# Kernel optimization log

Measured on AMD Instinct MI355X. Metric: run time of the kernel, lower is better.

The kernel has to match this reference:

```python
import jax, jax.numpy as jnp
import numpy as np

Q_PTS = jnp.array([0.0, 0.25, 0.5, 0.75, 1.0], dtype=jnp.float32)
LN_EPS = 1e-5


def _lower_median(s):
    # torch.median returns the LOWER of the two middle values for even n
    return s[..., (s.shape[-1] - 1) // 2]


def _quantile_sorted(s, q):
    # torch.quantile default 'linear' interpolation, computed on pre-sorted s
    n = s.shape[-1]
    idx = q * (n - 1)
    lo = jnp.floor(idx).astype(jnp.int32)
    hi = jnp.ceil(idx).astype(jnp.int32)
    frac = (idx - lo).astype(s.dtype)
    return jnp.take(s, lo, axis=-1) * (1.0 - frac) + jnp.take(s, hi, axis=-1) * frac


def _robust_stats(flat):
    # flat: [L-1, B, N] -> [L-1, B, 7]  (median, MAD, 5 quantiles)
    s = jnp.sort(flat, axis=-1)
    med = _lower_median(s)[..., None]
    mad = _lower_median(jnp.sort(jnp.abs(flat - med), axis=-1))[..., None]
    q = _quantile_sorted(s, Q_PTS)
    return jnp.concatenate([med, mad, q], axis=-1)


def _layer_norm(x, eps=LN_EPS):
    mu = x.mean(-1, keepdims=True)
    var = ((x - mu) ** 2).mean(-1, keepdims=True)
    return (x - mu) * jax.lax.rsqrt(var + eps)


def _forward(ws, bs, fc1_w, fc1_b, ln_w, ln_b, gate_w, gate_b, fco_w, fco_b, scale):
    Lm1, B = ws.shape[0], ws.shape[1]
    w_flat = ws.reshape(Lm1, B, -1)
    b_flat = bs.reshape(Lm1, B, -1)
    w_feats = _robust_stats(w_flat)            # [L-1, B, 7]
    b_feats = _robust_stats(b_flat)            # [L-1, B, 7]
    g_mean = w_flat.mean(-1, keepdims=True)    # [L-1, B, 1]
    g_mad = jnp.zeros_like(g_mean)             # MAD over a size-1 axis is exactly 0
    combined = jnp.concatenate([w_feats, b_feats, g_mean, g_mad], axis=-1)  # [L-1, B, 16]
    x = _layer_norm(combined)                  # F.layer_norm without affine
    # ResidualMLP (vectorized over the layer axis l)
    h = jnp.einsum('lbi,lhi->lbh', x, fc1_w) + fc1_b[:, None, :]
    h = _layer_norm(h) * ln_w[:, None, :] + ln_b[:, None, :]
    h = jax.nn.gelu(h, approximate=False)      # nn.GELU() default = exact erf
    gate = jax.nn.sigmoid(jnp.einsum('lbh,lgh->lbg', h, gate_w) + gate_b[:, None, :])
    raw = jnp.einsum('lbg,log->lbo', h * gate, fco_w) + fco_b[:, None, :]
    return jnp.sin(raw) * scale[:, None, None] + 1.0   # [L-1, B, out_dim]


def setup_inputs() -> dict:
    key = jax.random.key(0)
    ks = jax.random.split(key, 8)
    Lm1, B, D, H, F_IN = 3, 64, 512, 64, 16
    return {
        'ws': jax.random.normal(ks[0], (Lm1, B, D, D), jnp.float32) * 0.05,
        'bs': jax.random.normal(ks[1], (Lm1, B, D), jnp.float32) * 0.05,
        'w_last': jax.random.normal(ks[2], (B, D, D), jnp.float32) * 0.05,
        'b_last': jax.random.normal(ks[3], (B, D), jnp.float32) * 0.05,
        'fc1_w': jax.random.normal(ks[4], (Lm1, H, F_IN), jnp.float32) * 0.2,
        'fc1_b': jnp.zeros((Lm1, H), jnp.float32),
        'ln_w': jnp.ones((Lm1, H), jnp.float32),
        'ln_b': jnp.zeros((Lm1, H), jnp.float32),
        'gate_w': jax.random.normal(ks[5], (Lm1, H, H), jnp.float32) * 0.15,
        'gate_b': jnp.zeros((Lm1, H), jnp.float32),
        'fco_w': jax.random.normal(ks[6], (Lm1, D, H), jnp.float32) * 0.1,
        'fco_b': jnp.zeros((Lm1, D), jnp.float32),
        'scale': jnp.full((Lm1,), 0.1, jnp.float32),
    }


def reference(ws, bs, w_last, b_last, fc1_w, fc1_b, ln_w, ln_b, gate_w, gate_b, fco_w, fco_b, scale):
    # w_last / b_last correspond to wsfeat[L-1]: received by forward but never used
    # (loop breaks at i == L-1), matching the torch module exactly.
    return _forward(ws, bs, fc1_w, fc1_b, ln_w, ln_b, gate_w, gate_b, fco_w, fco_b, scale)
```

## Files before the change

kernel.cpp:

```cpp
#include <hip/hip_runtime.h>
#include <cstdint>

#define NROW 192
#define NW   262144
#define NT   1024
#define QCAP 1024
#define SEGS_CAP 8192

__device__ __forceinline__ uint32_t mono(float x) {
    uint32_t u = __float_as_uint(x);
    return (u & 0x80000000u) ? ~u : (u | 0x80000000u);
}
__device__ __forceinline__ float unmono(uint32_t u) {
    uint32_t v = (u & 0x80000000u) ? (u & 0x7FFFFFFFu) : ~u;
    return __uint_as_float(v);
}
__device__ __forceinline__ int binof(float x, float lo, float s) {
    float d = (x - lo) * s;
    d = fminf(fmaxf(d, 0.0f), 4095.0f);
    return (int)d;
}

__device__ void block_select(const uint32_t* hist, int nb, uint32_t rank,
                             uint32_t* sbuf, volatile uint32_t* out, int tid) {
    int per = (nb + NT - 1) / NT;
    int base = tid * per;
    uint32_t s = 0;
    for (int i = 0; i < per; ++i) { int idx = base + i; if (idx < nb) s += hist[idx]; }
    uint32_t p = s;
    int lane = tid & 63;
    #pragma unroll
    for (int off = 1; off < 64; off <<= 1) {
        uint32_t v = __shfl_up(p, off);
        if (lane >= off) p += v;
    }
    int w = tid >> 6;
    if (lane == 63) sbuf[w] = p;
    __syncthreads();
    if (tid == 0) {
        uint32_t acc = 0;
        for (int i = 0; i < 16; ++i) { uint32_t t = sbuf[i]; sbuf[16 + i] = acc; acc += t; }
    }
    __syncthreads();
    uint32_t excl = sbuf[16 + w] + p - s;
    if (rank >= excl && rank < excl + s) {
        uint32_t rem = rank - excl;
        for (int i = 0; i < per; ++i) {
            int idx = base + i;
            if (idx >= nb) break;
            uint32_t c = hist[idx];
            if (rem < c) { out[0] = (uint32_t)idx; out[1] = rem; break; }
            rem -= c;
        }
    }
    __syncthreads();
}

__device__ uint32_t seg_select(const uint32_t* seg, uint32_t cnt, uint32_t rank,
                               uint32_t* hist2, uint32_t* sbuf,
                               volatile uint32_t* out2, int tid) {
    for (int i = tid; i < 2048; i += NT) hist2[i] = 0;
    __syncthreads();
    for (uint32_t i = tid; i < cnt; i += NT) atomicAdd(&hist2[seg[i] >> 21], 1u);
    __syncthreads();
    block_select(hist2, 2048, rank, sbuf, out2, tid);
    uint32_t b1 = out2[0], r1 = out2[1];
    __syncthreads();
    for (int i = tid; i < 2048; i += NT) hist2[i] = 0;
    __syncthreads();
    for (uint32_t i = tid; i < cnt; i += NT) {
        uint32_t k = seg[i];
        if ((k >> 21) == b1) atomicAdd(&hist2[(k >> 10) & 2047u], 1u);
    }
    __syncthreads();
    block_select(hist2, 2048, r1, sbuf, out2, tid);
    uint32_t b2 = out2[0], r2 = out2[1];
    __syncthreads();
    for (int i = tid; i < 1024; i += NT) hist2[i] = 0;
    __syncthreads();
    for (uint32_t i = tid; i < cnt; i += NT) {
        uint32_t k = seg[i];
        if ((k >> 21) == b1 && ((k >> 10) & 2047u) == b2)
            atomicAdd(&hist2[k & 1023u], 1u);
    }
    __syncthreads();
    block_select(hist2, 1024, r2, sbuf, out2, tid);
    uint32_t b3 = out2[0];
    __syncthreads();
    return (b1 << 21) + (b2 << 10) + b3;
}

__device__ uint32_t refine_global(const float4* p4, float med, int mode,
                                  uint32_t b1, uint32_t rem,
                                  uint32_t* hist2, uint32_t* sbuf,
                                  volatile uint32_t* out2, int tid) {
    for (int i = tid; i < 2048; i += NT) hist2[i] = 0;
    __syncthreads();
    for (int it = 0; it < 64; ++it) {
        float4 v = p4[tid + it * NT];
        float xs[4] = {v.x, v.y, v.z, v.w};
        #pragma unroll
        for (int c = 0; c < 4; ++c) {
            uint32_t u = mode ? __float_as_uint(fabsf(xs[c] - med)) : mono(xs[c]);
            if ((u >> 20) == b1) atomicAdd(&hist2[(u >> 9) & 2047u], 1u);
        }
    }
    __syncthreads();
    block_select(hist2, 2048, rem, sbuf, out2, tid);
    uint32_t b2 = out2[0], r2 = out2[1];
    __syncthreads();
    for (int i = tid; i < 512; i += NT) hist2[i] = 0;
    __syncthreads();
    for (int it = 0; it < 64; ++it) {
        float4 v = p4[tid + it * NT];
        float xs[4] = {v.x, v.y, v.z, v.w};
        #pragma unroll
        for (int c = 0; c < 4; ++c) {
            uint32_t u = mode ? __float_as_uint(fabsf(xs[c] - med)) : mono(xs[c]);
            if ((u >> 20) == b1 && ((u >> 9) & 2047u) == b2)
                atomicAdd(&hist2[u & 511u], 1u);
        }
    }
    __syncthreads();
    block_select(hist2, 512, r2, sbuf, out2, tid);
    uint32_t b3 = out2[0];
    __syncthreads();
    return (b1 << 20) + (b2 << 9) + b3;
}

__device__ void fb_path(const float4* p4, float* feat, int row,
                        uint32_t* hist, uint32_t* hist2, uint32_t* sbuf,
                        volatile uint32_t* out2, int tid) {
    const uint32_t RANK6[6] = {65535u, 65536u, 131071u, 131072u, 196607u, 196608u};
    for (int i = tid; i < 4096; i += NT) hist[i] = 0;
    __syncthreads();
    for (int it = 0; it < 64; ++it) {
        float4 v = p4[tid + it * NT];
        float xs[4] = {v.x, v.y, v.z, v.w};
        #pragma unroll
        for (int c = 0; c < 4; ++c) atomicAdd(&hist[mono(xs[c]) >> 20], 1u);
    }
    __syncthreads();
    uint32_t bins[6], rems[6];
    for (int k = 0; k < 6; ++k) {
        block_select(hist, 4096, RANK6[k], sbuf, out2, tid);
        bins[k] = out2[0]; rems[k] = out2[1];
        __syncthreads();
    }
    float svv[6];
    for (int k = 0; k < 6; ++k)
        svv[k] = unmono(refine_global(p4, 0.f, 0, bins[k], rems[k], hist2, sbuf, out2, tid));
    if (tid == 0) {
        float* f = feat + row * 16;
        f[0] = svv[2];
        f[3] = 0.25f * svv[0] + 0.75f * svv[1];
        f[4] = 0.5f  * (svv[2] + svv[3]);
        f[5] = 0.75f * svv[4] + 0.25f * svv[5];
    }
    float med = svv[2];
    __syncthreads();
    for (int i = tid; i < 4096; i += NT) hist[i] = 0;
    __syncthreads();
    for (int it = 0; it < 64; ++it) {
        float4 v = p4[tid + it * NT];
        float xs[4] = {v.x, v.y, v.z, v.w};
        #pragma unroll
        for (int c = 0; c < 4; ++c)
            atomicAdd(&hist[__float_as_uint(fabsf(xs[c] - med)) >> 20], 1u);
    }
    __syncthreads();
    block_select(hist, 4096, 131071u, sbuf, out2, tid);
    uint32_t mb = out2[0], mr = out2[1];
    __syncthreads();
    uint32_t mu = refine_global(p4, med, 1, mb, mr, hist2, sbuf, out2, tid);
    if (tid == 0) feat[row * 16 + 1] = __uint_as_float(mu);
}

__device__ __forceinline__ uint32_t Pv(const uint32_t* P, int k) {
    return (k >= 4096) ? (uint32_t)NW : P[k];
}
__device__ __forceinline__ uint32_t wup(float mL, float mR, float tau,
                                        float blo, float bsc, const uint32_t* P) {
    const int bR = binof(mR + tau, blo, bsc);
    const int bL = binof(mL - tau, blo, bsc);
    return Pv(P, bR + 1) - P[bL];
}
__device__ __forceinline__ uint32_t wlow(float mL, float mR, float tau,
                                         float blo, float bsc, const uint32_t* P) {
    const int bR = binof(mL + tau, blo, bsc);
    const int bL = binof(mR - tau, blo, bsc);
    const uint32_t a = P[bR];
    const uint32_t b = Pv(P, bL + 1);
    return (a > b) ? (a - b) : 0u;
}

__device__ void bitonic512g(float* a, int t2) {
    for (int k = 2; k <= 512; k <<= 1) {
        for (int j = k >> 1; j > 0; j >>= 1) {
            __syncthreads();
            for (int i = t2; i < 512; i += 256) {
                int ixj = i ^ j;
                if (ixj > i) {
                    float x = a[i], y = a[ixj];
                    bool up = ((i & k) == 0);
                    if ((x > y) == up) { a[i] = y; a[ixj] = x; }
                }
            }
        }
    }
    __syncthreads();
}

__global__ __launch_bounds__(NT) void stats_kernel(const float* __restrict__ wsrc,
                                                   const float* __restrict__ bsrc,
                                                   float* __restrict__ feat) {
    const int tid = threadIdx.x;
    __shared__ uint32_t hist[4096];
    __shared__ uint32_t sbuf[1024];
    __shared__ uint32_t segs[SEGS_CAP];
    __shared__ uint32_t ctrl[64];
    __shared__ float fctrl[8];

    if (blockIdx.x >= NROW) {
        const int g = tid >> 8, t2 = tid & 255;
        const int brow = (blockIdx.x - NROW) * 4 + g;
        float* a = ((float*)segs) + g * 512;
        float* d = ((float*)segs) + 2048 + g * 512;
        const float* p = bsrc + (size_t)brow * 512;
        for (int i = t2; i < 512; i += 256) a[i] = p[i];
        bitonic512g(a, t2);
        const float bmed = a[255];
        if (t2 == 0) {
            float* f = feat + brow * 16;
            f[7]  = bmed;
            f[9]  = a[0];
            f[10] = 0.25f * a[127] + 0.75f * a[128];
            f[11] = 0.5f  * (a[255] + a[256]);
            f[12] = 0.75f * a[383] + 0.25f * a[384];
            f[13] = a[511];
        }
        __syncthreads();
        for (int i = t2; i < 512; i += 256) d[i] = fabsf(a[i] - bmed);
        bitonic512g(d, t2);
        if (t2 == 0) feat[brow * 16 + 8] = d[255];
        return;
    }

    const int row = blockIdx.x;
    const float4* __restrict__ p4 = (const float4*)(wsrc + (size_t)row * NW);
    const int lane = tid & 63, wv = tid >> 6;
    float* fsb = (float*)sbuf;
    volatile uint32_t* out2 = (volatile uint32_t*)(ctrl + 62);

    {
        float smin = 1e30f, smax = -1e30f;
        #pragma unroll
        for (int k = 0; k < 8; ++k) {
            float4 v = p4[tid + k * NT];
            smin = fminf(smin, fminf(fminf(v.x, v.y), fminf(v.z, v.w)));
            smax = fmaxf(smax, fmaxf(fmaxf(v.x, v.y), fmaxf(v.z, v.w)));
        }
        #pragma unroll
        for (int off = 32; off > 0; off >>= 1) {
            smin = fminf(smin, __shfl_down(smin, off));
            smax = fmaxf(smax, __shfl_down(smax, off));
        }
        if (lane == 0) { fsb[wv * 2] = smin; fsb[wv * 2 + 1] = smax; }
        __syncthreads();
        if (tid == 0) {
            float mn = 1e30f, mx = -1e30f;
            for (int i = 0; i < 16; ++i) { mn = fminf(mn, fsb[i * 2]); mx = fmaxf(mx, fsb[i * 2 + 1]); }
            float span = mx - mn;
            float lo = mn - 0.0625f * span;
            float s = (span > 0.f) ? 4096.0f / (span * 1.125f) : 0.0f;
            fctrl[0] = lo; fctrl[1] = s;
        }
        __syncthreads();
    }
    const float blo = fctrl[0], bsc = fctrl[1];

    for (int i = tid; i < 4096; i += NT) hist[i] = 0;
    __syncthreads();
    {
        float sum = 0.f, fmn = 1e30f, fmx = -1e30f;
        for (int it = 0; it < 64; it += 8) {
            float4 a8[8];
            #pragma unroll
            for (int j = 0; j < 8; ++j) a8[j] = p4[tid + (it + j) * NT];
            #pragma unroll
            for (int j = 0; j < 8; ++j) {
                float xs[4] = {a8[j].x, a8[j].y, a8[j].z, a8[j].w};
                #pragma unroll
                for (int c = 0; c < 4; ++c) {
                    float x = xs[c];
                    sum += x;
                    fmn = fminf(fmn, x);
                    fmx = fmaxf(fmx, x);
                    atomicAdd(&hist[binof(x, blo, bsc)], 1u);
                }
            }
        }
        #pragma unroll
        for (int off = 32; off > 0; off >>= 1) {
            sum += __shfl_down(sum, off);
            fmn = fminf(fmn, __shfl_down(fmn, off));
            fmx = fmaxf(fmx, __shfl_down(fmx, off));
        }
        __syncthreads();
        if (lane == 0) { fsb[wv * 4] = sum; fsb[wv * 4 + 1] = fmn; fsb[wv * 4 + 2] = fmx; }
        __syncthreads();
        if (tid == 0) { float s = 0; for (int i = 0; i < 16; ++i) s += fsb[i * 4]; feat[row * 16 + 14] = s * (1.0f / (float)NW); }
        if (tid == 1) { float m = 1e30f;  for (int i = 0; i < 16; ++i) m = fminf(m, fsb[i * 4 + 1]); feat[row * 16 + 2] = m; fctrl[2] = m; }
        if (tid == 2) { float M = -1e30f; for (int i = 0; i < 16; ++i) M = fmaxf(M, fsb[i * 4 + 2]); feat[row * 16 + 6] = M; fctrl[3] = M; }
        if (tid == 3) feat[row * 16 + 15] = 0.0f;
        __syncthreads();
    }

    {
        const int b4 = tid * 4;
        const uint32_t v0 = hist[b4], v1 = hist[b4 + 1], v2 = hist[b4 + 2], v3 = hist[b4 + 3];
        const uint32_t s = v0 + v1 + v2 + v3;
        uint32_t p = s;
        #pragma unroll
        for (int off = 1; off < 64; off <<= 1) {
            uint32_t t = __shfl_up(p, off);
            if (lane >= off) p += t;
        }
        if (lane == 63) sbuf[wv] = p;
        __syncthreads();
        if (tid == 0) {
            uint32_t acc = 0;
            for (int i = 0; i < 16; ++i) { uint32_t t = sbuf[i]; sbuf[16 + i] = acc; acc += t; }
        }
        __syncthreads();
        const uint32_t excl = sbuf[16 + wv] + p - s;
        uint32_t ppA[5];
        ppA[0] = excl; ppA[1] = excl + v0; ppA[2] = ppA[1] + v1; ppA[3] = ppA[2] + v2; ppA[4] = ppA[3] + v3;
        hist[b4] = ppA[0]; hist[b4 + 1] = ppA[1]; hist[b4 + 2] = ppA[2]; hist[b4 + 3] = ppA[3];
        const uint32_t RANKS[6] = {65535u, 65536u, 131071u, 131072u, 196607u, 196608u};
        #pragma unroll
        for (int c = 0; c < 4; ++c) {
            #pragma unroll
            for (int q = 0; q < 6; ++q) {
                const uint32_t r = RANKS[q];
                if (ppA[c] <= r && r < ppA[c + 1]) {
                    ctrl[12 + q] = (uint32_t)(b4 + c);
                    ctrl[18 + q] = r - ppA[c];
                    ctrl[48 + q] = ppA[c + 1] - ppA[c];
                }
            }
        }
        __syncthreads();
    }

    if (tid == 0) {
        uint32_t ndl = 0, fail = 0;
        #pragma unroll
        for (int q = 0; q < 6; ++q) {
            const uint32_t b = ctrl[12 + q];
            int jf = -1;
            for (uint32_t t = 0; t < ndl; ++t) if (ctrl[24 + t] == b) { jf = (int)t; break; }
            if (jf < 0) {
                jf = (int)ndl;
                ctrl[24 + ndl] = b;
                ctrl[30 + ndl] = ctrl[48 + q];
                ndl++;
            }
            ctrl[36 + q] = (uint32_t)jf;
        }
        uint32_t off = 0;
        for (uint32_t t = 0; t < ndl; ++t) {
            ctrl[54 + t] = off;
            if (ctrl[30 + t] > QCAP) fail = 1;
            off += ctrl[30 + t];
        }
        if (off > 6144u) fail = 1;
        if (ctrl[14] == 0u || ctrl[14] == 4095u) fail = 1;
        ctrl[60] = off;
        ctrl[10] = ndl;
        ctrl[11] = fail;
        #pragma unroll
        for (int j = 0; j < 6; ++j) ctrl[j] = 0;
        ctrl[6] = 0;
        ctrl[7] = 0;
        ctrl[8] = 0;
        ctrl[9] = 0;
        ctrl[48] = 0xFFFFFFFFu; ctrl[49] = 0xFFFFFFFFu;
    }
    __syncthreads();
    if (ctrl[11]) { fb_path(p4, feat, row, hist, segs, sbuf, out2, tid); return; }

    const float wbin = 1.0f / bsc;
    const uint32_t m0 = ctrl[14];

    sbuf[tid] = 0;
    {
        const float mLf = blo + (float)m0 * wbin;
        const float mRf = mLf + wbin;
        #pragma unroll
        for (int c = 0; c < 4; ++c) {
            const int j = tid * 4 + c;
            const float tau = (float)j * wbin;
            const uint32_t up_j = wup(mLf, mRf, tau, blo, bsc, hist);
            if (up_j <= 131071u) {
                bool bnd = (j == 4095);
                if (!bnd) bnd = (wup(mLf, mRf, (float)(j + 1) * wbin, blo, bsc, hist) > 131071u);
                if (bnd) ctrl[48] = (uint32_t)j;
            }
            const uint32_t lo_j = wlow(mLf, mRf, tau, blo, bsc, hist);
            if (lo_j >= 131072u) {
                bool bnd = (j == 0);
                if (!bnd) bnd = (wlow(mLf, mRf, (float)(j - 1) * wbin, blo, bsc, hist) < 131072u);
                if (bnd) ctrl[49] = (uint32_t)j;
            }
        }
    }
    __syncthreads();
    if (tid < (int)ctrl[10]) ((uint8_t*)sbuf)[ctrl[24 + tid]] = (uint8_t)(tid + 1);
    const uint32_t jlo = ctrl[48], jhi = ctrl[49];
    float Awin = -1.0f;
    if (jlo != 0xFFFFFFFFu && jlo >= 2u) Awin = (float)(jlo - 2u) * wbin;
    float Bwin = (jhi == 0xFFFFFFFFu) ? 3.0e38f : (float)(jhi + 3u) * wbin;
    Bwin = fmaxf(Bwin, Awin + 3.0f * wbin);
    const float mtld = blo + ((float)m0 + 0.5f) * wbin;
    const uint32_t madbase = ctrl[60];
    __syncthreads();

    uint32_t myclo = 0;
    {
        const uint8_t* tbl = (const uint8_t*)sbuf;
        for (int it = 0; it < 64; it += 8) {
            float4 a8[8];
            #pragma unroll
            for (int j = 0; j < 8; ++j) a8[j] = p4[tid + (it + j) * NT];
            #pragma unroll
            for (int j = 0; j < 8; ++j) {
                float xs[4] = {a8[j].x, a8[j].y, a8[j].z, a8[j].w};
                #pragma unroll
                for (int c = 0; c < 4; ++c) {
                    float x = xs[c];
                    uint32_t m = tbl[binof(x, blo, bsc)];
                    if (m) {
                        uint32_t jj = m - 1u;
                        uint32_t pos = atomicAdd(&ctrl[jj], 1u);
                        if (pos < ctrl[30 + jj]) segs[ctrl[54 + jj] + pos] = mono(x);
                    }
                    float u = fabsf(x - mtld);
                    if (u <= Awin) myclo++;
                    else if (u <= Bwin) {
                        uint32_t pos = atomicAdd(&ctrl[6], 1u);
                        uint32_t slot = madbase + pos;
                        if (slot < SEGS_CAP) segs[slot] = __float_as_uint(x);
                    }
                }
            }
        }
    }
    __syncthreads();
    #pragma unroll
    for (int off = 32; off > 0; off >>= 1) myclo += __shfl_down(myclo, off);
    if (lane == 0) sbuf[wv] = myclo;
    __syncthreads();
    if (tid == 0) {
        uint32_t clo = 0;
        for (int i = 0; i < 16; ++i) clo += sbuf[i];
        ctrl[7] = clo;
        uint32_t fail = 0;
        const uint32_t ndl = ctrl[10];
        for (uint32_t j = 0; j < ndl; ++j) if (ctrl[j] != ctrl[30 + j]) fail = 1;
        if (ctrl[6] > SEGS_CAP - madbase) fail = 1;
        ctrl[11] = fail;
    }
    __syncthreads();
    if (ctrl[11]) { fb_path(p4, feat, row, hist, segs, sbuf, out2, tid); return; }

    {
        const uint32_t ndl = ctrl[10];
        for (uint32_t j = 0; j < ndl; ++j) {
            const uint32_t cnt = ctrl[j];
            const uint32_t base = ctrl[54 + j];
            if ((uint32_t)tid < cnt) {
                const uint32_t key = segs[base + tid];
                uint32_t r = 0;
                for (uint32_t i = 0; i < cnt; ++i) {
                    const uint32_t ki = segs[base + i];
                    r += (ki < key || (ki == key && i < (uint32_t)tid)) ? 1u : 0u;
                }
                #pragma unroll
                for (int q = 0; q < 6; ++q)
                    if (ctrl[36 + q] == j && ctrl[18 + q] == r) ctrl[42 + q] = key;
            }
        }
    }
    __syncthreads();
    const float med = unmono(ctrl[44]);
    if (tid == 0) {
        float* f = feat + row * 16;
        f[0] = med;
        f[3] = 0.25f * unmono(ctrl[42]) + 0.75f * unmono(ctrl[43]);
        f[4] = 0.5f  * (med + unmono(ctrl[45]));
        f[5] = 0.75f * unmono(ctrl[46]) + 0.25f * unmono(ctrl[47]);
    }

    const uint32_t mcnt = ctrl[6];
    const float thq = Awin + wbin;
    const float tcq = Bwin - 2.0f * wbin;
    uint32_t n2t = 0, n2c = 0;
    for (uint32_t i = (uint32_t)tid; i < mcnt; i += NT) {
        float x = __uint_as_float(segs[madbase + i]);
        float t = fabsf(x - med);
        segs[madbase + i] = __float_as_uint(t);
        n2t += (t <= thq) ? 1u : 0u;
        n2c += (t <= tcq) ? 1u : 0u;
    }
    #pragma unroll
    for (int off = 32; off > 0; off >>= 1) {
        n2t += __shfl_down(n2t, off);
        n2c += __shfl_down(n2c, off);
    }
    if (lane == 0) { atomicAdd(&ctrl[8], n2t); atomicAdd(&ctrl[9], n2c); }
    __syncthreads();
    if (tid == 0) {
        const uint32_t clo = ctrl[7];
        uint32_t fail = 0;
        if (clo > 131071u) fail = 1;
        if (clo + ctrl[8] > 131071u) fail = 1;
        if (clo + ctrl[9] < 131072u) fail = 1;
        if (!fail && (131071u - clo) >= mcnt) fail = 1;
        ctrl[11] = fail;
    }
    __syncthreads();
    if (ctrl[11]) { fb_path(p4, feat, row, hist, segs, sbuf, out2, tid); return; }
    const uint32_t kR = 131071u - ctrl[7];
    uint32_t madu = seg_select(segs + madbase, mcnt, kR, hist, sbuf, out2, tid);
    if (tid == 0) feat[row * 16 + 1] = __uint_as_float(madu);
}

__global__ __launch_bounds__(256) void mlp_kernel(
    const float* __restrict__ feat,
    const float* __restrict__ fc1_w, const float* __restrict__ fc1_b,
    const float* __restrict__ ln_w,  const float* __restrict__ ln_b,
    const float* __restrict__ gate_w, const float* __restrict__ gate_b,
    const float* __restrict__ fco_w,  const float* __restrict__ fco_b,
    const float* __restrict__ scale,  float* __restrict__ out) {
    const int row = blockIdx.x;
    const int tid = threadIdx.x;
    const int l = row >> 6;
    __shared__ float x[16], h[64], hg[64], stats[2];

    if (tid < 16) x[tid] = feat[row * 16 + tid];
    __syncthreads();

    if (tid == 0) {
        float mu = 0.f;
        for (int i = 0; i < 16; ++i) mu += x[i];
        mu *= (1.f / 16.f);
        float var = 0.f;
        for (int i = 0; i < 16; ++i) { float dd = x[i] - mu; var += dd * dd; }
        var *= (1.f / 16.f);
        stats[0] = mu; stats[1] = rsqrtf(var + 1e-5f);
    }
    __syncthreads();
    if (tid < 16) x[tid] = (x[tid] - stats[0]) * stats[1];
    __syncthreads();
    if (tid < 64) {
        const float* wv = fc1_w + ((size_t)l * 64 + tid) * 16;
        float acc = fc1_b[l * 64 + tid];
        #pragma unroll
        for (int i = 0; i < 16; ++i) acc += x[i] * wv[i];
        h[tid] = acc;
    }
    __syncthreads();
    if (tid == 0) {
        float mu = 0.f;
        for (int i = 0; i < 64; ++i) mu += h[i];
        mu *= (1.f / 64.f);
        float var = 0.f;
        for (int i = 0; i < 64; ++i) { float dd = h[i] - mu; var += dd * dd; }
        var *= (1.f / 64.f);
        stats[0] = mu; stats[1] = rsqrtf(var + 1e-5f);
    }
    __syncthreads();
    if (tid < 64) {
        float v = (h[tid] - stats[0]) * stats[1] * ln_w[l * 64 + tid] + ln_b[l * 64 + tid];
        h[tid] = 0.5f * v * (1.0f + erff(v * 0.70710678118654752f));
    }
    __syncthreads();
    if (tid < 64) {
        const float* wv = gate_w + ((size_t)l * 64 + tid) * 64;
        float acc = gate_b[l * 64 + tid];
        #pragma unroll
        for (int i = 0; i < 64; ++i) acc += h[i] * wv[i];
        float g = 1.0f / (1.0f + expf(-acc));
        hg[tid] = h[tid] * g;
    }
    __syncthreads();
    const float sc = scale[l];
    for (int o = tid; o < 512; o += 256) {
        const float* wv = fco_w + ((size_t)l * 512 + o) * 64;
        float acc = fco_b[l * 512 + o];
        #pragma unroll
        for (int i = 0; i < 64; ++i) acc += hg[i] * wv[i];
        out[(size_t)row * 512 + o] = sinf(acc) * sc + 1.0f;
    }
}

extern "C" void kernel_launch(void* const* d_in, const int* in_sizes, int n_in,
                              void* d_out, int out_size, void* d_ws, size_t ws_size,
                              hipStream_t stream) {
    const float* ws_in  = (const float*)d_in[0];
    const float* bs_in  = (const float*)d_in[1];
    const float* fc1_w  = (const float*)d_in[4];
    const float* fc1_b  = (const float*)d_in[5];
    const float* ln_w   = (const float*)d_in[6];
    const float* ln_b   = (const float*)d_in[7];
    const float* gate_w = (const float*)d_in[8];
    const float* gate_b = (const float*)d_in[9];
    const float* fco_w  = (const float*)d_in[10];
    const float* fco_b  = (const float*)d_in[11];
    const float* scale  = (const float*)d_in[12];
    float* out  = (float*)d_out;
    float* feat = (float*)d_ws;

    hipLaunchKernelGGL(stats_kernel, dim3(NROW + NROW / 4), dim3(NT), 0, stream,
                       ws_in, bs_in, feat);
    hipLaunchKernelGGL(mlp_kernel, dim3(NROW), dim3(256), 0, stream,
                       feat, fc1_w, fc1_b, ln_w, ln_b, gate_w, gate_b,
                       fco_w, fco_b, scale, out);
}
```

Before: 413.7 us.

## Fuse bias stats, weight stats and MLP into one kernel per row

New measurement: 424.3 us. 2.6% more time.

```diff
diff --git a/kernel.cpp b/kernel.cpp
--- a/kernel.cpp
+++ b/kernel.cpp
@@ -5,7 +5,7 @@
 #define NW   262144
 #define NT   1024
 #define QCAP 1024
-#define SEGS_CAP 8192
+#define SEGS_CAP 12288
 
 __device__ __forceinline__ uint32_t mono(float x) {
     uint32_t u = __float_as_uint(x);
@@ -128,7 +128,7 @@
     return (b1 << 20) + (b2 << 9) + b3;
 }
 
-__device__ void fb_path(const float4* p4, float* feat, int row,
+__device__ void fb_path(const float4* p4, float* xf,
                         uint32_t* hist, uint32_t* hist2, uint32_t* sbuf,
                         volatile uint32_t* out2, int tid) {
     const uint32_t RANK6[6] = {65535u, 65536u, 131071u, 131072u, 196607u, 196608u};
@@ -151,11 +151,10 @@
     for (int k = 0; k < 6; ++k)
         svv[k] = unmono(refine_global(p4, 0.f, 0, bins[k], rems[k], hist2, sbuf, out2, tid));
     if (tid == 0) {
-        float* f = feat + row * 16;
-        f[0] = svv[2];
-        f[3] = 0.25f * svv[0] + 0.75f * svv[1];
-        f[4] = 0.5f  * (svv[2] + svv[3]);
-        f[5] = 0.75f * svv[4] + 0.25f * svv[5];
+        xf[0] = svv[2];
+        xf[3] = 0.25f * svv[0] + 0.75f * svv[1];
+        xf[4] = 0.5f  * (svv[2] + svv[3]);
+        xf[5] = 0.75f * svv[4] + 0.25f * svv[5];
     }
     float med = svv[2];
     __syncthreads();
@@ -173,7 +172,7 @@
     uint32_t mb = out2[0], mr = out2[1];
     __syncthreads();
     uint32_t mu = refine_global(p4, med, 1, mb, mr, hist2, sbuf, out2, tid);
-    if (tid == 0) feat[row * 16 + 1] = __uint_as_float(mu);
+    if (tid == 0) xf[1] = __uint_as_float(mu);
 }
 
 __device__ __forceinline__ uint32_t Pv(const uint32_t* P, int k) {
@@ -194,12 +193,12 @@
     return (a > b) ? (a - b) : 0u;
 }
 
-__device__ void bitonic512g(float* a, int t2) {
+__device__ void bitonic512w(float* a, int tid) {
     for (int k = 2; k <= 512; k <<= 1) {
         for (int j = k >> 1; j > 0; j >>= 1) {
             __syncthreads();
-            for (int i = t2; i < 512; i += 256) {
-                int ixj = i ^ j;
+            if (tid < 512) {
+                int i = tid, ixj = i ^ j;
                 if (ixj > i) {
                     float x = a[i], y = a[ixj];
                     bool up = ((i & k) == 0);
@@ -211,43 +210,10 @@
     __syncthreads();
 }
 
-__global__ __launch_bounds__(NT) void stats_kernel(const float* __restrict__ wsrc,
-                                                   const float* __restrict__ bsrc,
-                                                   float* __restrict__ feat) {
-    const int tid = threadIdx.x;
-    __shared__ uint32_t hist[4096];
-    __shared__ uint32_t sbuf[1024];
-    __shared__ uint32_t segs[SEGS_CAP];
-    __shared__ uint32_t ctrl[64];
-    __shared__ float fctrl[8];
-
-    if (blockIdx.x >= NROW) {
-        const int g = tid >> 8, t2 = tid & 255;
-        const int brow = (blockIdx.x - NROW) * 4 + g;
-        float* a = ((float*)segs) + g * 512;
-        float* d = ((float*)segs) + 2048 + g * 512;
-        const float* p = bsrc + (size_t)brow * 512;
-        for (int i = t2; i < 512; i += 256) a[i] = p[i];
-        bitonic512g(a, t2);
-        const float bmed = a[255];
-        if (t2 == 0) {
-            float* f = feat + brow * 16;
-            f[7]  = bmed;
-            f[9]  = a[0];
-            f[10] = 0.25f * a[127] + 0.75f * a[128];
-            f[11] = 0.5f  * (a[255] + a[256]);
-            f[12] = 0.75f * a[383] + 0.25f * a[384];
-            f[13] = a[511];
-        }
-        __syncthreads();
-        for (int i = t2; i < 512; i += 256) d[i] = fabsf(a[i] - bmed);
-        bitonic512g(d, t2);
-        if (t2 == 0) feat[brow * 16 + 8] = d[255];
-        return;
-    }
-
-    const int row = blockIdx.x;
-    const float4* __restrict__ p4 = (const float4*)(wsrc + (size_t)row * NW);
+__device__ void wstats_body(const float4* __restrict__ p4, float* xf,
+                            uint32_t* hist, uint32_t* histB,
+                            uint32_t* sbuf, uint32_t* segs,
+                            uint32_t* ctrl, float* fctrl, int tid) {
     const int lane = tid & 63, wv = tid >> 6;
     float* fsb = (float*)sbuf;
     volatile uint32_t* out2 = (volatile uint32_t*)(ctrl + 62);
@@ -279,9 +245,10 @@
     }
     const float blo = fctrl[0], bsc = fctrl[1];
 
-    for (int i = tid; i < 4096; i += NT) hist[i] = 0;
+    for (int i = tid; i < 4096; i += NT) { hist[i] = 0; histB[i] = 0; }
     __syncthreads();
     {
+        uint32_t* hsel = (wv & 1) ? histB : hist;
         float sum = 0.f, fmn = 1e30f, fmx = -1e30f;
         for (int it = 0; it < 64; it += 8) {
             float4 a8[8];
@@ -296,7 +263,7 @@
                     sum += x;
                     fmn = fminf(fmn, x);
                     fmx = fmaxf(fmx, x);
-                    atomicAdd(&hist[binof(x, blo, bsc)], 1u);
+                    atomicAdd(&hsel[binof(x, blo, bsc)], 1u);
                 }
             }
         }
@@ -309,10 +276,12 @@
         __syncthreads();
         if (lane == 0) { fsb[wv * 4] = sum; fsb[wv * 4 + 1] = fmn; fsb[wv * 4 + 2] = fmx; }
         __syncthreads();
-        if (tid == 0) { float s = 0; for (int i = 0; i < 16; ++i) s += fsb[i * 4]; feat[row * 16 + 14] = s * (1.0f / (float)NW); }
-        if (tid == 1) { float m = 1e30f;  for (int i = 0; i < 16; ++i) m = fminf(m, fsb[i * 4 + 1]); feat[row * 16 + 2] = m; fctrl[2] = m; }
-        if (tid == 2) { float M = -1e30f; for (int i = 0; i < 16; ++i) M = fmaxf(M, fsb[i * 4 + 2]); feat[row * 16 + 6] = M; fctrl[3] = M; }
-        if (tid == 3) feat[row * 16 + 15] = 0.0f;
+        if (tid == 0) { float s = 0; for (int i = 0; i < 16; ++i) s += fsb[i * 4]; xf[14] = s * (1.0f / (float)NW); }
+        if (tid == 1) { float m = 1e30f;  for (int i = 0; i < 16; ++i) m = fminf(m, fsb[i * 4 + 1]); xf[2] = m; fctrl[2] = m; }
+        if (tid == 2) { float M = -1e30f; for (int i = 0; i < 16; ++i) M = fmaxf(M, fsb[i * 4 + 2]); xf[6] = M; fctrl[3] = M; }
+        if (tid == 3) xf[15] = 0.0f;
+        __syncthreads();
+        for (int i = tid; i < 4096; i += NT) hist[i] += histB[i];
         __syncthreads();
     }
 
@@ -388,7 +357,7 @@
         ctrl[48] = 0xFFFFFFFFu; ctrl[49] = 0xFFFFFFFFu;
     }
     __syncthreads();
-    if (ctrl[11]) { fb_path(p4, feat, row, hist, segs, sbuf, out2, tid); return; }
+    if (ctrl[11]) { fb_path(p4, xf, hist, segs, sbuf, out2, tid); return; }
 
     const float wbin = 1.0f / bsc;
     const uint32_t m0 = ctrl[14];
@@ -472,7 +441,7 @@
         ctrl[11] = fail;
     }
     __syncthreads();
-    if (ctrl[11]) { fb_path(p4, feat, row, hist, segs, sbuf, out2, tid); return; }
+    if (ctrl[11]) { fb_path(p4, xf, hist, segs, sbuf, out2, tid); return; }
 
     {
         const uint32_t ndl = ctrl[10];
@@ -495,11 +464,10 @@
     __syncthreads();
     const float med = unmono(ctrl[44]);
     if (tid == 0) {
-        float* f = feat + row * 16;
-        f[0] = med;
-        f[3] = 0.25f * unmono(ctrl[42]) + 0.75f * unmono(ctrl[43]);
-        f[4] = 0.5f  * (med + unmono(ctrl[45]));
-        f[5] = 0.75f * unmono(ctrl[46]) + 0.25f * unmono(ctrl[47]);
+        xf[0] = med;
+        xf[3] = 0.25f * unmono(ctrl[42]) + 0.75f * unmono(ctrl[43]);
+        xf[4] = 0.5f  * (med + unmono(ctrl[45]));
+        xf[5] = 0.75f * unmono(ctrl[46]) + 0.25f * unmono(ctrl[47]);
     }
 
     const uint32_t mcnt = ctrl[6];
@@ -530,14 +498,14 @@
         ctrl[11] = fail;
     }
     __syncthreads();
-    if (ctrl[11]) { fb_path(p4, feat, row, hist, segs, sbuf, out2, tid); return; }
+    if (ctrl[11]) { fb_path(p4, xf, hist, segs, sbuf, out2, tid); return; }
     const uint32_t kR = 131071u - ctrl[7];
     uint32_t madu = seg_select(segs + madbase, mcnt, kR, hist, sbuf, out2, tid);
-    if (tid == 0) feat[row * 16 + 1] = __uint_as_float(madu);
-}
-
-__global__ __launch_bounds__(256) void mlp_kernel(
-    const float* __restrict__ feat,
+    if (tid == 0) xf[1] = __uint_as_float(madu);
+}
+
+__global__ __launch_bounds__(NT) void fused_kernel(
+    const float* __restrict__ wsrc, const float* __restrict__ bsrc,
     const float* __restrict__ fc1_w, const float* __restrict__ fc1_b,
     const float* __restrict__ ln_w,  const float* __restrict__ ln_b,
     const float* __restrict__ gate_w, const float* __restrict__ gate_b,
@@ -546,57 +514,86 @@
     const int row = blockIdx.x;
     const int tid = threadIdx.x;
     const int l = row >> 6;
-    __shared__ float x[16], h[64], hg[64], stats[2];
-
-    if (tid < 16) x[tid] = feat[row * 16 + tid];
+    __shared__ uint32_t hist[4096];
+    __shared__ uint32_t histB[4096];
+    __shared__ uint32_t sbuf[1024];
+    __shared__ uint32_t segs[SEGS_CAP];
+    __shared__ uint32_t ctrl[64];
+    __shared__ float fctrl[8];
+    __shared__ float xf[16], hm[64], hg[64], st2[2];
+
+    {
+        float* a = (float*)segs;
+        float* d = ((float*)segs) + 512;
+        const float* p = bsrc + (size_t)row * 512;
+        if (tid < 512) a[tid] = p[tid];
+        bitonic512w(a, tid);
+        const float bmed = a[255];
+        if (tid == 0) {
+            xf[7]  = bmed;
+            xf[9]  = a[0];
+            xf[10] = 0.25f * a[127] + 0.75f * a[128];
+            xf[11] = 0.5f  * (a[255] + a[256]);
+            xf[12] = 0.75f * a[383] + 0.25f * a[384];
+            xf[13] = a[511];
+        }
+        __syncthreads();
+        if (tid < 512) d[tid] = fabsf(a[tid] - bmed);
+        bitonic512w(d, tid);
+        if (tid == 0) xf[8] = d[255];
+        __syncthreads();
+    }
+
+    wstats_body((const float4*)(wsrc + (size_t)row * NW), xf,
+                hist, histB, sbuf, segs, ctrl, fctrl, tid);
     __syncthreads();
 
     if (tid == 0) {
         float mu = 0.f;
-        for (int i = 0; i < 16; ++i) mu += x[i];
+        for (int i = 0; i < 16; ++i) mu += xf[i];
         mu *= (1.f / 16.f);
         float var = 0.f;
-        for (int i = 0; i < 16; ++i) { float dd = x[i] - mu; var += dd * dd; }
+        for (int i = 0; i < 16; ++i) { float dd = xf[i] - mu; var += dd * dd; }
         var *= (1.f / 16.f);
-        stats[0] = mu; stats[1] = rsqrtf(var + 1e-5f);
-    }
-    __syncthreads();
-    if (tid < 16) x[tid] = (x[tid] - stats[0]) * stats[1];
+        st2[0] = mu; st2[1] = rsqrtf(var + 1e-5f);
+    }
+    __syncthreads();
+    if (tid < 16) xf[tid] = (xf[tid] - st2[0]) * st2[1];
     __syncthreads();
     if (tid < 64) {
         const float* wv = fc1_w + ((size_t)l * 64 + tid) * 16;
         float acc = fc1_b[l * 64 + tid];
         #pragma unroll
-        for (int i = 0; i < 16; ++i) acc += x[i] * wv[i];
-        h[tid] = acc;
+        for (int i = 0; i < 16; ++i) acc += xf[i] * wv[i];
+        hm[tid] = acc;
     }
     __syncthreads();
     if (tid == 0) {
         float mu = 0.f;
-        for (int i = 0; i < 64; ++i) mu += h[i];
+        for (int i = 0; i < 64; ++i) mu += hm[i];
         mu *= (1.f / 64.f);
         float var = 0.f;
-        for (int i = 0; i < 64; ++i) { float dd = h[i] - mu; var += dd * dd; }
+        for (int i = 0; i < 64; ++i) { float dd = hm[i] - mu; var += dd * dd; }
         var *= (1.f / 64.f);
-        stats[0] = mu; stats[1] = rsqrtf(var + 1e-5f);
+        st2[0] = mu; st2[1] = rsqrtf(var + 1e-5f);
     }
     __syncthreads();
     if (tid < 64) {
-        float v = (h[tid] - stats[0]) * stats[1] * ln_w[l * 64 + tid] + ln_b[l * 64 + tid];
-        h[tid] = 0.5f * v * (1.0f + erff(v * 0.70710678118654752f));
+        float v = (hm[tid] - st2[0]) * st2[1] * ln_w[l * 64 + tid] + ln_b[l * 64 + tid];
+        hm[tid] = 0.5f * v * (1.0f + erff(v * 0.70710678118654752f));
     }
     __syncthreads();
     if (tid < 64) {
         const float* wv = gate_w + ((size_t)l * 64 + tid) * 64;
         float acc = gate_b[l * 64 + tid];
         #pragma unroll
-        for (int i = 0; i < 64; ++i) acc += h[i] * wv[i];
+        for (int i = 0; i < 64; ++i) acc += hm[i] * wv[i];
         float g = 1.0f / (1.0f + expf(-acc));
-        hg[tid] = h[tid] * g;
+        hg[tid] = hm[tid] * g;
     }
     __syncthreads();
     const float sc = scale[l];
-    for (int o = tid; o < 512; o += 256) {
+    for (int o = tid; o < 512; o += NT) {
         const float* wv = fco_w + ((size_t)l * 512 + o) * 64;
         float acc = fco_b[l * 512 + o];
         #pragma unroll
@@ -620,11 +617,8 @@
     const float* fco_b  = (const float*)d_in[11];
     const float* scale  = (const float*)d_in[12];
     float* out  = (float*)d_out;
-    float* feat = (float*)d_ws;
-
-    hipLaunchKernelGGL(stats_kernel, dim3(NROW + NROW / 4), dim3(NT), 0, stream,
-                       ws_in, bs_in, feat);
-    hipLaunchKernelGGL(mlp_kernel, dim3(NROW), dim3(256), 0, stream,
-                       feat, fc1_w, fc1_b, ln_w, ln_b, gate_w, gate_b,
+
+    hipLaunchKernelGGL(fused_kernel, dim3(NROW), dim3(NT), 0, stream,
+                       ws_in, bs_in, fc1_w, fc1_b, ln_w, ln_b, gate_w, gate_b,
                        fco_w, fco_b, scale, out);
 }
```
